# Optimization experiments

Hardware: AMD Instinct MI355X
Metric: run time of the kernel (lower is better)

## Reference

```python
import jax, jax.numpy as jnp
import numpy as np

# few-shot episode constants (from args: 5-way 5-shot, 15 query shots, resnet backbone)
WAY, SHOT, QUERY_SHOT = 5, 5, 15
D, M = 640, 25            # channels, h*w of resnet12 feature map
G, Q = 4, 5               # group-selection hyperparams (used only as scalar normalizers in live path)


def setup_inputs() -> dict:
    key = jax.random.key(0)
    k1, k2 = jax.random.split(key)
    n = WAY * SHOT + WAY * QUERY_SHOT          # 100 images per episode
    feature_map = jax.random.normal(k1, (n, D, M), dtype=jnp.float32)
    # SCIW spatial weights: [way*shot, query_num, m]
    weight2 = jax.random.uniform(k2, (WAY * SHOT, WAY * QUERY_SHOT, M), dtype=jnp.float32)
    scale = jnp.ones((1,), dtype=jnp.float32)  # nn.Parameter([1.0])
    return {"feature_map": feature_map, "weight2": weight2, "scale": scale}


def reference(feature_map, weight2, scale):
    ns = WAY * SHOT
    support = feature_map[:ns]     # [S, D, M]  (way*shot flattened, viewed back as way*shot,d,m)
    query = feature_map[ns:]       # [Qn, D, M]
    # Original: p_c = support[S,1,D,M] * weight2[S,Qn,1,M]; centroid = p_c.mean(-1)
    #           p_q = query[1,Qn,D,M] * weight2[S,Qn,1,M]; query   = p_q.mean(-1)
    # Fused as einsum contractions over m (same math, no 4D materialization).
    centroid = jnp.einsum('sdm,sqm->sqd', support, weight2) / M   # [S, Qn, D]
    query_r = jnp.einsum('qdm,sqm->sqd', query, weight2) / M      # [S, Qn, D]
    l2 = jnp.sum((centroid - query_r) ** 2, axis=-1)              # [S, Qn]
    neg_l2 = -l2.T                                                # [Qn, S]
    logits = neg_l2 / (G * Q * Q * SHOT) * scale                  # broadcast scalar param
    return jax.nn.log_softmax(logits, axis=1)
```

## Files before the change

kernel.cpp:

```cpp
#include <hip/hip_runtime.h>
#include <math.h>

#define NS 25
#define NQ 75
#define DDIM 640
#define MDIM 25
#define MP 26
#define NPAIR 1875

__global__ __launch_bounds__(256) void l2_kernel(
    const float* __restrict__ fm, const float* __restrict__ w2,
    const float* __restrict__ scale, float* __restrict__ logits)
{
    int orig = blockIdx.x;
    const int qch = NPAIR / 8;
    const int r   = NPAIR % 8;
    int xcd  = orig & 7;
    int base = (xcd < r) ? xcd * (qch + 1) : r * (qch + 1) + (xcd - r) * qch;
    int wgid = base + (orig >> 3);
    int q = wgid / NS;
    int s = wgid % NS;

    __shared__ float Slds[256 * MP];
    __shared__ float Qlds[256 * MP];
    __shared__ float red[4];

    int tid = threadIdx.x;

    float w[MDIM];
    const float* wp = w2 + (s * NQ + q) * MDIM;
    #pragma unroll
    for (int m = 0; m < MDIM; ++m) w[m] = wp[m];

    const float* Sg = fm + (size_t)s * (DDIM * MDIM);
    const float* Qg = fm + (size_t)(NS + q) * (DDIM * MDIM);

    float partial = 0.f;

    for (int base_d = 0; base_d < DDIM; base_d += 256) {
        int len  = min(256, DDIM - base_d);
        int n4   = (len * MDIM) / 4;
        const float4* S4 = (const float4*)(Sg + base_d * MDIM);
        const float4* Q4 = (const float4*)(Qg + base_d * MDIM);
        for (int i = tid; i < n4; i += 256) {
            float4 v = S4[i];
            float4 u = Q4[i];
            int idx = 4 * i;
            #pragma unroll
            for (int k = 0; k < 4; ++k) {
                int dd = (idx + k) / MDIM, mm = (idx + k) % MDIM;
                Slds[dd * MP + mm] = (&v.x)[k];
                Qlds[dd * MP + mm] = (&u.x)[k];
            }
        }
        __syncthreads();
        if (tid < len) {
            const float* Sr = Slds + tid * MP;
            const float* Qr = Qlds + tid * MP;
            float acc = 0.f;
            #pragma unroll
            for (int m = 0; m < MDIM; ++m)
                acc += (Sr[m] - Qr[m]) * w[m];
            partial += acc * acc;
        }
        __syncthreads();
    }

    #pragma unroll
    for (int off = 32; off >= 1; off >>= 1)
        partial += __shfl_xor(partial, off, 64);
    if ((tid & 63) == 0) red[tid >> 6] = partial;
    __syncthreads();
    if (tid == 0) {
        float tot = red[0] + red[1] + red[2] + red[3];
        logits[q * NS + s] = -tot * (1.0f / 312500.0f) * scale[0];
    }
}

__global__ __launch_bounds__(64) void lsm_kernel(const float* __restrict__ logits,
                                                float* __restrict__ out)
{
    int q = blockIdx.x;
    int t = threadIdx.x;
    float x = (t < NS) ? logits[q * NS + t] : -INFINITY;
    float mx = x;
    #pragma unroll
    for (int off = 32; off >= 1; off >>= 1)
        mx = fmaxf(mx, __shfl_xor(mx, off, 64));
    float e = (t < NS) ? expf(x - mx) : 0.f;
    float sum = e;
    #pragma unroll
    for (int off = 32; off >= 1; off >>= 1)
        sum += __shfl_xor(sum, off, 64);
    if (t < NS) out[q * NS + t] = x - mx - logf(sum);
}

extern "C" void kernel_launch(void* const* d_in, const int* in_sizes, int n_in,
                              void* d_out, int out_size, void* d_ws, size_t ws_size,
                              hipStream_t stream) {
    const float* fm    = (const float*)d_in[0];
    const float* w2    = (const float*)d_in[1];
    const float* scale = (const float*)d_in[2];
    float* logits = (float*)d_ws;
    float* out    = (float*)d_out;

    l2_kernel<<<NPAIR, 256, 0, stream>>>(fm, w2, scale, logits);
    lsm_kernel<<<NQ, 64, 0, stream>>>(logits, out);
}
```

Baseline: 86.94 us.

## Tile support×query pairs 5x5 per block with D-chunk split and atomic reduction

```diff
diff --git a/kernel.cpp b/kernel.cpp
--- a/kernel.cpp
+++ b/kernel.cpp
@@ -5,84 +5,92 @@
 #define NQ 75
 #define DDIM 640
 #define MDIM 25
-#define MP 26
-#define NPAIR 1875
+#define SLICE (DDIM*MDIM)
+#define CHUNK_D 64
+#define CHUNK_F (CHUNK_D*MDIM)
+#define ST 5
+#define QT 15
+#define DC 10
+#define NBLK (ST*QT*DC)
 
-__global__ __launch_bounds__(256) void l2_kernel(
-    const float* __restrict__ fm, const float* __restrict__ w2,
-    const float* __restrict__ scale, float* __restrict__ logits)
+__global__ __launch_bounds__(320) void l2_kernel(const float* __restrict__ fm,
+                                                 const float* __restrict__ w2,
+                                                 float* __restrict__ raw)
 {
-    int orig = blockIdx.x;
-    const int qch = NPAIR / 8;
-    const int r   = NPAIR % 8;
-    int xcd  = orig & 7;
-    int base = (xcd < r) ? xcd * (qch + 1) : r * (qch + 1) + (xcd - r) * qch;
-    int wgid = base + (orig >> 3);
-    int q = wgid / NS;
-    int s = wgid % NS;
+    __shared__ float Sl[5 * CHUNK_F];
+    __shared__ float Ql[5 * CHUNK_F];
 
-    __shared__ float Slds[256 * MP];
-    __shared__ float Qlds[256 * MP];
-    __shared__ float red[4];
+    int b = blockIdx.x;
+    const int q8 = NBLK / 8, r8 = NBLK % 8;
+    int xcd = b & 7;
+    int wg = ((xcd < r8) ? xcd * (q8 + 1) : r8 * (q8 + 1) + (xcd - r8) * q8) + (b >> 3);
+    int dc = wg % DC;
+    int pq = wg / DC;
+    int qt = pq % QT, st = pq / QT;
+    int s0 = st * 5, q0 = qt * 5;
 
-    int tid = threadIdx.x;
+    int tid  = threadIdx.x;
+    int si   = __builtin_amdgcn_readfirstlane(tid >> 6);
+    int lane = tid & 63;
 
-    float w[MDIM];
-    const float* wp = w2 + (s * NQ + q) * MDIM;
+    const float* sg = fm + (size_t)(s0 + si) * SLICE + dc * CHUNK_F;
+    const float* qg = fm + (size_t)(NS + q0 + si) * SLICE + dc * CHUNK_F;
+    float* sl = Sl + si * CHUNK_F;
+    float* ql = Ql + si * CHUNK_F;
     #pragma unroll
-    for (int m = 0; m < MDIM; ++m) w[m] = wp[m];
+    for (int i = 0; i < 6; ++i) {
+        __builtin_amdgcn_global_load_lds(
+            (const __attribute__((address_space(1))) void*)(sg + i * 256 + lane * 4),
+            (__attribute__((address_space(3))) void*)(sl + i * 256), 16, 0, 0);
+        __builtin_amdgcn_global_load_lds(
+            (const __attribute__((address_space(1))) void*)(qg + i * 256 + lane * 4),
+            (__attribute__((address_space(3))) void*)(ql + i * 256), 16, 0, 0);
+    }
+    __builtin_amdgcn_global_load_lds(
+        (const __attribute__((address_space(1))) void*)(sg + 1536 + lane),
+        (__attribute__((address_space(3))) void*)(sl + 1536), 4, 0, 0);
+    __builtin_amdgcn_global_load_lds(
+        (const __attribute__((address_space(1))) void*)(qg + 1536 + lane),
+        (__attribute__((address_space(3))) void*)(ql + 1536), 4, 0, 0);
 
-    const float* Sg = fm + (size_t)s * (DDIM * MDIM);
-    const float* Qg = fm + (size_t)(NS + q) * (DDIM * MDIM);
+    __syncthreads();
 
-    float partial = 0.f;
+    float srow[MDIM];
+    const float* srp = Sl + si * CHUNK_F + lane * MDIM;
+    #pragma unroll
+    for (int m = 0; m < MDIM; ++m) srow[m] = srp[m];
 
-    for (int base_d = 0; base_d < DDIM; base_d += 256) {
-        int len  = min(256, DDIM - base_d);
-        int n4   = (len * MDIM) / 4;
-        const float4* S4 = (const float4*)(Sg + base_d * MDIM);
-        const float4* Q4 = (const float4*)(Qg + base_d * MDIM);
-        for (int i = tid; i < n4; i += 256) {
-            float4 v = S4[i];
-            float4 u = Q4[i];
-            int idx = 4 * i;
-            #pragma unroll
-            for (int k = 0; k < 4; ++k) {
-                int dd = (idx + k) / MDIM, mm = (idx + k) % MDIM;
-                Slds[dd * MP + mm] = (&v.x)[k];
-                Qlds[dd * MP + mm] = (&u.x)[k];
-            }
-        }
-        __syncthreads();
-        if (tid < len) {
-            const float* Sr = Slds + tid * MP;
-            const float* Qr = Qlds + tid * MP;
-            float acc = 0.f;
-            #pragma unroll
-            for (int m = 0; m < MDIM; ++m)
-                acc += (Sr[m] - Qr[m]) * w[m];
-            partial += acc * acc;
-        }
-        __syncthreads();
+    float acc[5];
+    #pragma unroll
+    for (int qi = 0; qi < 5; ++qi) {
+        const float* wp = w2 + ((size_t)(s0 + si) * NQ + (q0 + qi)) * MDIM;
+        const float* qrp = Ql + qi * CHUNK_F + lane * MDIM;
+        float a = 0.f;
+        #pragma unroll
+        for (int m = 0; m < MDIM; ++m)
+            a = fmaf(srow[m] - qrp[m], wp[m], a);
+        acc[qi] = a * a;
     }
 
     #pragma unroll
-    for (int off = 32; off >= 1; off >>= 1)
-        partial += __shfl_xor(partial, off, 64);
-    if ((tid & 63) == 0) red[tid >> 6] = partial;
-    __syncthreads();
-    if (tid == 0) {
-        float tot = red[0] + red[1] + red[2] + red[3];
-        logits[q * NS + s] = -tot * (1.0f / 312500.0f) * scale[0];
+    for (int qi = 0; qi < 5; ++qi) {
+        float v = acc[qi];
+        #pragma unroll
+        for (int off = 32; off >= 1; off >>= 1)
+            v += __shfl_xor(v, off, 64);
+        if (lane == 0)
+            atomicAdd(&raw[(q0 + qi) * NS + (s0 + si)], v);
     }
 }
 
-__global__ __launch_bounds__(64) void lsm_kernel(const float* __restrict__ logits,
-                                                float* __restrict__ out)
+__global__ __launch_bounds__(64) void lsm_kernel(const float* __restrict__ raw,
+                                                 const float* __restrict__ scale,
+                                                 float* __restrict__ out)
 {
     int q = blockIdx.x;
     int t = threadIdx.x;
-    float x = (t < NS) ? logits[q * NS + t] : -INFINITY;
+    float sc = scale[0] * (-1.0f / 312500.0f);
+    float x = (t < NS) ? raw[q * NS + t] * sc : -INFINITY;
     float mx = x;
     #pragma unroll
     for (int off = 32; off >= 1; off >>= 1)
@@ -101,9 +109,10 @@
     const float* fm    = (const float*)d_in[0];
     const float* w2    = (const float*)d_in[1];
     const float* scale = (const float*)d_in[2];
-    float* logits = (float*)d_ws;
-    float* out    = (float*)d_out;
+    float* raw = (float*)d_ws;
+    float* out = (float*)d_out;
 
-    l2_kernel<<<NPAIR, 256, 0, stream>>>(fm, w2, scale, logits);
-    lsm_kernel<<<NQ, 64, 0, stream>>>(logits, out);
+    hipMemsetAsync(raw, 0, NQ * NS * sizeof(float), stream);
+    l2_kernel<<<NBLK, 320, 0, stream>>>(fm, w2, raw);
+    lsm_kernel<<<NQ, 64, 0, stream>>>(raw, scale, out);
 }
```

Result: faster. 83.92 us (-3.5%).
